# Kernel optimization log

Measured on AMD Instinct MI355X. Metric: run time of the kernel, lower is better.

## Reference

```python
import jax, jax.numpy as jnp
import numpy as np

N = 50000      # n_nodes
E = 800000     # n_edges (avg degree 16)
D_IN, D_HID, D_OUT = 128, 128, 64


def setup_inputs() -> dict:
    key = jax.random.key(0)
    ks = jax.random.split(key, 6)
    x = jax.random.normal(ks[0], (N, D_IN), dtype=jnp.float32)
    edge_index = jax.random.randint(ks[1], (2, E), 0, N, dtype=jnp.int32)
    # GCNConv params (glorot-ish scale), bias enabled by default in PyG
    W1 = jax.random.normal(ks[2], (D_IN, D_HID), dtype=jnp.float32) * (1.0 / np.sqrt(D_IN))
    b1 = jnp.zeros((D_HID,), dtype=jnp.float32)
    W2 = jax.random.normal(ks[3], (D_HID, D_OUT), dtype=jnp.float32) * (1.0 / np.sqrt(D_HID))
    b2 = jnp.zeros((D_OUT,), dtype=jnp.float32)
    return {"x": x, "edge_index": edge_index, "W1": W1, "b1": b1, "W2": W2, "b2": b2}


def _gcn_conv(x, src, dst, W, b):
    """PyG GCNConv: linear transform, add self-loops (weight 1),
    symmetric D^-1/2 A D^-1/2 aggregation (source->target), add bias."""
    xw = x @ W                                                # [N, Dout]
    ones = jnp.ones(dst.shape[0], dtype=xw.dtype)
    deg = jax.ops.segment_sum(ones, dst, num_segments=N) + 1.0  # +1 self-loop
    dis = jax.lax.rsqrt(deg)                                  # deg >= 1
    norm = dis[src] * dis[dst]                                # [E]
    msg = xw[src] * norm[:, None]                             # gather + scale
    agg = jax.ops.segment_sum(msg, dst, num_segments=N)       # scatter-add
    agg = agg + xw * (dis * dis)[:, None]                     # self-loop term
    return agg + b


def reference(x, edge_index, W1, b1, W2, b2):
    src, dst = edge_index[0], edge_index[1]
    z = jax.nn.relu(_gcn_conv(x, src, dst, W1, b1))
    z = _gcn_conv(z, src, dst, W2, b2)
    return z
```

## Files before the change

### kernel.cpp

```cpp
#include <hip/hip_runtime.h>

#define NN 50000
#define NE 800000
#define NB 196
#define BCAP 4608
#define KPAD 136
#define WSLAB (2 * 64 * KPAD)
#define CHUNKS 782
#define G1A 391
#define NBF 256

typedef __bf16 bf16x8 __attribute__((ext_vector_type(8)));
typedef float  f32x4  __attribute__((ext_vector_type(4)));

static __device__ __forceinline__ float bf2f(unsigned short h){
  union { unsigned u; float f; } c; c.u = ((unsigned)h) << 16; return c.f;
}
static __device__ __forceinline__ unsigned short f2bf(float f){
  union { float f; unsigned u; } c; c.f = f;
  unsigned u = c.u;
  return (unsigned short)((u + 0x7fffu + ((u >> 16) & 1u)) >> 16);
}
static __device__ __forceinline__ void split8(const float* f, bf16x8& hi, bf16x8& lo){
  #pragma unroll
  for (int j = 0; j < 8; j++){
    __bf16 h = (__bf16)f[j];
    hi[j] = h;
    lo[j] = (__bf16)(f[j] - (float)h);
  }
}
static __device__ __forceinline__ void addu4s(float* a, uint4 w, float s){
  a[0] = fmaf(s, bf2f((unsigned short)(w.x & 0xffffu)), a[0]);
  a[1] = fmaf(s, bf2f((unsigned short)(w.x >> 16)),     a[1]);
  a[2] = fmaf(s, bf2f((unsigned short)(w.y & 0xffffu)), a[2]);
  a[3] = fmaf(s, bf2f((unsigned short)(w.y >> 16)),     a[3]);
  a[4] = fmaf(s, bf2f((unsigned short)(w.z & 0xffffu)), a[4]);
  a[5] = fmaf(s, bf2f((unsigned short)(w.z >> 16)),     a[5]);
  a[6] = fmaf(s, bf2f((unsigned short)(w.w & 0xffffu)), a[6]);
  a[7] = fmaf(s, bf2f((unsigned short)(w.w >> 16)),     a[7]);
}
static __device__ __forceinline__ void addu4(float* a, uint4 w){
  a[0] += bf2f((unsigned short)(w.x & 0xffffu)); a[1] += bf2f((unsigned short)(w.x >> 16));
  a[2] += bf2f((unsigned short)(w.y & 0xffffu)); a[3] += bf2f((unsigned short)(w.y >> 16));
  a[4] += bf2f((unsigned short)(w.z & 0xffffu)); a[5] += bf2f((unsigned short)(w.z >> 16));
  a[6] += bf2f((unsigned short)(w.w & 0xffffu)); a[7] += bf2f((unsigned short)(w.w >> 16));
}

static __device__ __forceinline__ void gemm1_body(int chunk, int t,
    const float* __restrict__ X, const unsigned short* __restrict__ wbuf,
    unsigned short* __restrict__ Y){
  const int wv = t >> 6;
  const int lane = t & 63;
  const int m = lane & 15;
  const int quad = lane >> 4;
  const int R0 = chunk * 64;
  const int row = R0 + wv * 16 + m;
  const int rowc = min(row, NN - 1);
  const float* pX = X + (size_t)rowc * 128 + quad * 8;

  f32x4 acc[8];
  #pragma unroll
  for (int tt = 0; tt < 8; tt++) acc[tt] = (f32x4){0.f, 0.f, 0.f, 0.f};

  #pragma unroll
  for (int ki = 0; ki < 4; ki++){
    float a[8];
    *(float4*)(a)     = *(const float4*)(pX + ki * 32);
    *(float4*)(a + 4) = *(const float4*)(pX + ki * 32 + 4);
    bf16x8 ah, al;
    split8(a, ah, al);
    #pragma unroll
    for (int tt = 0; tt < 8; tt++){
      const unsigned short* bp = wbuf + (tt >> 2) * WSLAB
                               + ((tt & 3) * 16 + m) * KPAD + ki * 32 + quad * 8;
      bf16x8 bh = *(const bf16x8*)bp;
      bf16x8 bl = *(const bf16x8*)(bp + 64 * KPAD);
      acc[tt] = __builtin_amdgcn_mfma_f32_16x16x32_bf16(ah, bh, acc[tt], 0, 0, 0);
      acc[tt] = __builtin_amdgcn_mfma_f32_16x16x32_bf16(ah, bl, acc[tt], 0, 0, 0);
      acc[tt] = __builtin_amdgcn_mfma_f32_16x16x32_bf16(al, bh, acc[tt], 0, 0, 0);
    }
  }

  const int orow = R0 + wv * 16 + quad * 4;
  #pragma unroll
  for (int r = 0; r < 4; r++){
    int gr = orow + r;
    if (gr < NN){
      #pragma unroll
      for (int tt = 0; tt < 8; tt++)
        Y[(size_t)gr * 128 + (tt >> 2) * 64 + (tt & 3) * 16 + m] = f2bf(acc[tt][r]);
    }
  }
}

__global__ __launch_bounds__(256) void k_prep(const float* __restrict__ W1,
    const float* __restrict__ W2, unsigned short* __restrict__ wbuf,
    int* __restrict__ gcur){
  int s = blockIdx.x;
  if (s == 3){
    if (threadIdx.x < NB) gcur[threadIdx.x] = 0;
    return;
  }
  const float* W = (s < 2) ? W1 : W2;
  int ldw = (s < 2) ? 128 : 64;
  int coff = (s == 1) ? 64 : 0;
  unsigned short* wh = wbuf + (size_t)s * WSLAB;
  unsigned short* wl = wh + 64 * KPAD;
  for (int i = threadIdx.x; i < 128 * 64; i += 256){
    int k = i >> 6, n = i & 63;
    float v = W[(size_t)k * ldw + coff + n];
    unsigned short h = f2bf(v);
    unsigned short l = f2bf(v - bf2f(h));
    wh[n * KPAD + k] = h;
    wl[n * KPAD + k] = l;
  }
}

__global__ __launch_bounds__(256) void k_fg1(const int* __restrict__ src,
    const int* __restrict__ dst, int* __restrict__ gcur, unsigned* __restrict__ stg,
    const float* __restrict__ X, const unsigned short* __restrict__ wbuf,
    unsigned short* __restrict__ Y){
  const int bid = blockIdx.x;
  const int t = threadIdx.x;
  if (bid >= NBF){
    gemm1_body(bid - NBF, t, X, wbuf, Y);
    return;
  }
  __shared__ int lcnt[NB];
  __shared__ int gbase[NB];
  for (int i = t; i < NB; i += 256) lcnt[i] = 0;
  __syncthreads();
  const int per = (NE + NBF - 1) / NBF;
  const int e0 = bid * per, e1 = min(e0 + per, NE);
  for (int e = e0 + t; e < e1; e += 256)
    atomicAdd(&lcnt[dst[e] >> 8], 1);
  __syncthreads();
  for (int b = t; b < NB; b += 256){
    gbase[b] = atomicAdd(&gcur[b], lcnt[b]);
    lcnt[b] = 0;
  }
  __syncthreads();
  for (int e = e0 + t; e < e1; e += 256){
    int d = dst[e];
    int b = d >> 8;
    unsigned entry = (unsigned)src[e] | (((unsigned)d & 255u) << 16);
    int pos = gbase[b] + atomicAdd(&lcnt[b], 1);
    if (pos < BCAP) stg[(size_t)b * BCAP + pos] = entry;
  }
}

__global__ __launch_bounds__(256) void k_bg1(const unsigned* __restrict__ stg,
    const int* __restrict__ gcur, int* __restrict__ rowstart, int* __restrict__ cnt,
    float* __restrict__ dis, int* __restrict__ csr,
    const float* __restrict__ X, const unsigned short* __restrict__ wbuf,
    unsigned short* __restrict__ Y){
  const int bid = blockIdx.x;
  const int t = threadIdx.x;
  if (bid >= NB){
    gemm1_body(G1A + (bid - NB), t, X, wbuf, Y);
    return;
  }
  __shared__ int lcnt[256];
  __shared__ int sm[256];
  const int b = bid;
  const int ecnt = min(gcur[b], BCAP);
  const int ebase = b * BCAP;
  lcnt[t] = 0;
  __syncthreads();
  for (int i = t; i < ecnt; i += 256){
    unsigned en = stg[ebase + i];
    atomicAdd(&lcnt[(en >> 16) & 255u], 1);
  }
  __syncthreads();
  int v = lcnt[t];
  sm[t] = v;
  __syncthreads();
  #pragma unroll
  for (int off = 1; off < 256; off <<= 1){
    int x = (t >= off) ? sm[t - off] : 0;
    __syncthreads();
    sm[t] += x;
    __syncthreads();
  }
  const int loff = sm[t] - v;
  const int node = (b << 8) + t;
  if (node < NN){
    rowstart[node] = ebase + loff;
    cnt[node] = v;
    dis[node] = rsqrtf((float)v + 1.0f);
  }
  __syncthreads();
  lcnt[t] = loff;
  __syncthreads();
  for (int i = t; i < ecnt; i += 256){
    unsigned en = stg[ebase + i];
    int pos = atomicAdd(&lcnt[(en >> 16) & 255u], 1);
    csr[ebase + pos] = (int)(en & 0xffffu);
  }
}

__global__ __launch_bounds__(256) void k_agg1(const unsigned short* __restrict__ Y,
    const int* __restrict__ rowstart, const int* __restrict__ cnt,
    const int* __restrict__ csr, const float* __restrict__ dis,
    const float* __restrict__ bias, unsigned short* __restrict__ OH){
  const int n = (blockIdx.x * 256 + threadIdx.x) >> 6;
  const int lane = threadIdx.x & 63;
  const int q = lane >> 4;
  const int l = lane & 15;
  if (n >= NN) return;
  const float dn = dis[n];
  float a[8] = {0.f, 0.f, 0.f, 0.f, 0.f, 0.f, 0.f, 0.f};
  if (q == 0)
    addu4s(a, *(const uint4*)(Y + (size_t)n * 128 + (l << 3)), dn);
  const int start = rowstart[n];
  const int end = start + cnt[n];
  int i = start;
  for (; i + 16 <= end; i += 16){
    int s0 = csr[i + q],     s1 = csr[i + 4 + q];
    int s2 = csr[i + 8 + q], s3 = csr[i + 12 + q];
    float d0 = dis[s0], d1 = dis[s1], d2 = dis[s2], d3 = dis[s3];
    uint4 w0 = *(const uint4*)(Y + (size_t)s0 * 128 + (l << 3));
    uint4 w1 = *(const uint4*)(Y + (size_t)s1 * 128 + (l << 3));
    uint4 w2 = *(const uint4*)(Y + (size_t)s2 * 128 + (l << 3));
    uint4 w3 = *(const uint4*)(Y + (size_t)s3 * 128 + (l << 3));
    addu4s(a, w0, d0); addu4s(a, w1, d1); addu4s(a, w2, d2); addu4s(a, w3, d3);
  }
  for (; i + 8 <= end; i += 8){
    int s0 = csr[i + q], s1 = csr[i + 4 + q];
    float d0 = dis[s0], d1 = dis[s1];
    uint4 w0 = *(const uint4*)(Y + (size_t)s0 * 128 + (l << 3));
    uint4 w1 = *(const uint4*)(Y + (size_t)s1 * 128 + (l << 3));
    addu4s(a, w0, d0); addu4s(a, w1, d1);
  }
  for (; i < end; i += 4){
    int idx = i + q;
    if (idx < end){
      int s = csr[idx];
      addu4s(a, *(const uint4*)(Y + (size_t)s * 128 + (l << 3)), dis[s]);
    }
  }
  #pragma unroll
  for (int j = 0; j < 8; j++){
    a[j] += __shfl_xor(a[j], 16);
    a[j] += __shfl_xor(a[j], 32);
  }
  if (q == 0){
    float bi[8];
    *(float4*)(bi)     = *(const float4*)(bias + (l << 3));
    *(float4*)(bi + 4) = *(const float4*)(bias + (l << 3) + 4);
    unsigned hv[4];
    #pragma unroll
    for (int j = 0; j < 4; j++){
      float o0 = fmaxf(dn * a[2 * j]     + bi[2 * j],     0.f);
      float o1 = fmaxf(dn * a[2 * j + 1] + bi[2 * j + 1], 0.f);
      hv[j] = (unsigned)f2bf(o0) | ((unsigned)f2bf(o1) << 16);
    }
    *(uint4*)(OH + (size_t)n * 128 + (l << 3)) = make_uint4(hv[0], hv[1], hv[2], hv[3]);
  }
}

__global__ __launch_bounds__(256) void k_gemm2(const unsigned short* __restrict__ Ah,
    const unsigned short* __restrict__ Wsl, const float* __restrict__ dis,
    unsigned short* __restrict__ Y){
  const int t = threadIdx.x;
  const int wv = t >> 6;
  const int lane = t & 63;
  const int m = lane & 15;
  const int quad = lane >> 4;
  const int R0 = blockIdx.x * 64;
  const int row = R0 + wv * 16 + m;
  const int rowc = min(row, NN - 1);
  const unsigned short* pAh = Ah + (size_t)rowc * 128 + quad * 8;

  f32x4 acc[4];
  #pragma unroll
  for (int tt = 0; tt < 4; tt++) acc[tt] = (f32x4){0.f, 0.f, 0.f, 0.f};

  #pragma unroll
  for (int ki = 0; ki < 4; ki++){
    bf16x8 ah = *(const bf16x8*)(pAh + ki * 32);
    #pragma unroll
    for (int tt = 0; tt < 4; tt++){
      const unsigned short* bp = Wsl + (tt * 16 + m) * KPAD + ki * 32 + quad * 8;
      bf16x8 bh = *(const bf16x8*)bp;
      bf16x8 bl = *(const bf16x8*)(bp + 64 * KPAD);
      acc[tt] = __builtin_amdgcn_mfma_f32_16x16x32_bf16(ah, bh, acc[tt], 0, 0, 0);
      acc[tt] = __builtin_amdgcn_mfma_f32_16x16x32_bf16(ah, bl, acc[tt], 0, 0, 0);
    }
  }

  const int orow = R0 + wv * 16 + quad * 4;
  #pragma unroll
  for (int r = 0; r < 4; r++){
    int gr = orow + r;
    if (gr < NN){
      float dsc = dis[gr];
      #pragma unroll
      for (int tt = 0; tt < 4; tt++)
        Y[(size_t)gr * 64 + tt * 16 + m] = f2bf(acc[tt][r] * dsc);
    }
  }
}

__global__ __launch_bounds__(256) void k_agg64(const unsigned short* __restrict__ Y,
    const int* __restrict__ rowstart, const int* __restrict__ cnt,
    const int* __restrict__ csr, const float* __restrict__ dis,
    const float* __restrict__ bias, float* __restrict__ OUT){
  const int n = (blockIdx.x * 256 + threadIdx.x) >> 6;
  const int lane = threadIdx.x & 63;
  const int g = lane >> 3;
  const int l = lane & 7;
  if (n >= NN) return;
  float a[8] = {0.f, 0.f, 0.f, 0.f, 0.f, 0.f, 0.f, 0.f};
  if (g == 0)
    addu4(a, *(const uint4*)(Y + (size_t)n * 64 + (l << 3)));
  const int start = rowstart[n];
  const int end = start + cnt[n];
  int i = start;
  for (; i + 16 <= end; i += 16){
    int s0 = csr[i + g], s1 = csr[i + 8 + g];
    uint4 w0 = *(const uint4*)(Y + (size_t)s0 * 64 + (l << 3));
    uint4 w1 = *(const uint4*)(Y + (size_t)s1 * 64 + (l << 3));
    addu4(a, w0); addu4(a, w1);
  }
  for (; i < end; i += 8){
    int idx = i + g;
    if (idx < end){
      int s = csr[idx];
      addu4(a, *(const uint4*)(Y + (size_t)s * 64 + (l << 3)));
    }
  }
  #pragma unroll
  for (int j = 0; j < 8; j++){
    a[j] += __shfl_xor(a[j], 8);
    a[j] += __shfl_xor(a[j], 16);
    a[j] += __shfl_xor(a[j], 32);
  }
  if (g == 0){
    const float dn = dis[n];
    float bi[8];
    *(float4*)(bi)     = *(const float4*)(bias + (l << 3));
    *(float4*)(bi + 4) = *(const float4*)(bias + (l << 3) + 4);
    float4 o0, o1;
    o0.x = dn * a[0] + bi[0]; o0.y = dn * a[1] + bi[1];
    o0.z = dn * a[2] + bi[2]; o0.w = dn * a[3] + bi[3];
    o1.x = dn * a[4] + bi[4]; o1.y = dn * a[5] + bi[5];
    o1.z = dn * a[6] + bi[6]; o1.w = dn * a[7] + bi[7];
    *(float4*)(OUT + (size_t)n * 64 + (l << 3))     = o0;
    *(float4*)(OUT + (size_t)n * 64 + (l << 3) + 4) = o1;
  }
}

extern "C" void kernel_launch(void* const* d_in, const int* in_sizes, int n_in,
                              void* d_out, int out_size, void* d_ws, size_t ws_size,
                              hipStream_t stream) {
  const float* x  = (const float*)d_in[0];
  const int*   ei = (const int*)d_in[1];
  const int*   src = ei;
  const int*   dst = ei + NE;
  const float* W1 = (const float*)d_in[2];
  const float* b1 = (const float*)d_in[3];
  const float* W2 = (const float*)d_in[4];
  const float* b2 = (const float*)d_in[5];
  float* out = (float*)d_out;

  char* w = (char*)d_ws;
  auto alloc = [&](size_t bytes){ void* p = (void*)w; w += (bytes + 255) & ~(size_t)255; return p; };
  int*   gcur     = (int*)alloc(NB * 4);
  int*   rowstart = (int*)alloc((size_t)NN * 4);
  int*   cnt      = (int*)alloc((size_t)NN * 4);
  float* dis      = (float*)alloc((size_t)NN * 4);
  unsigned* stg   = (unsigned*)alloc((size_t)NB * BCAP * 4);
  int*   csr      = (int*)alloc((size_t)NB * BCAP * 4);
  unsigned short* y1 = (unsigned short*)alloc((size_t)NN * 128 * 2);
  unsigned short* hh = (unsigned short*)alloc((size_t)NN * 128 * 2);
  unsigned short* y2 = (unsigned short*)alloc((size_t)NN * 64 * 2);
  unsigned short* wbuf = (unsigned short*)alloc((size_t)3 * WSLAB * 2);

  const int AGG_BLOCKS = (NN * 64 + 255) / 256;
  unsigned short* wsl2 = wbuf + (size_t)2 * WSLAB;

  k_prep<<<4, 256, 0, stream>>>(W1, W2, wbuf, gcur);
  k_fg1 <<<NBF + G1A, 256, 0, stream>>>(src, dst, gcur, stg, x, wbuf, y1);
  k_bg1 <<<NB + (CHUNKS - G1A), 256, 0, stream>>>(stg, gcur, rowstart, cnt, dis, csr,
                                                  x, wbuf, y1);
  k_agg1 <<<AGG_BLOCKS, 256, 0, stream>>>(y1, rowstart, cnt, csr, dis, b1, hh);
  k_gemm2<<<CHUNKS, 256, 0, stream>>>(hh, wsl2, dis, y2);
  k_agg64<<<AGG_BLOCKS, 256, 0, stream>>>(y2, rowstart, cnt, csr, dis, b2, out);
}
```

Baseline: 196.2 us.

## Fuse layer-1 aggregation into layer-2 GEMM via shared-memory tile

Merges the first-layer neighbor aggregation (with bias and ReLU) and the second-layer MFMA GEMM into one kernel. Each block aggregates 64 nodes into a bf16 tile in LDS, then runs the GEMM straight from LDS. This removes one launch and the global write and read of the 50000x128 hidden buffer. In exchange the grid drops to 782 blocks, each doing 16 serial aggregation iterations per wave, which reduces parallelism and latency hiding for the gather-heavy aggregation.

```diff
diff --git a/kernel.cpp b/kernel.cpp
--- a/kernel.cpp
+++ b/kernel.cpp
@@ -199,86 +199,92 @@
   }
 }
 
-__global__ __launch_bounds__(256) void k_agg1(const unsigned short* __restrict__ Y,
+__global__ __launch_bounds__(256) void k_aggemm2(const unsigned short* __restrict__ Y,
     const int* __restrict__ rowstart, const int* __restrict__ cnt,
     const int* __restrict__ csr, const float* __restrict__ dis,
-    const float* __restrict__ bias, unsigned short* __restrict__ OH){
-  const int n = (blockIdx.x * 256 + threadIdx.x) >> 6;
-  const int lane = threadIdx.x & 63;
-  const int q = lane >> 4;
-  const int l = lane & 15;
-  if (n >= NN) return;
-  const float dn = dis[n];
-  float a[8] = {0.f, 0.f, 0.f, 0.f, 0.f, 0.f, 0.f, 0.f};
-  if (q == 0)
-    addu4s(a, *(const uint4*)(Y + (size_t)n * 128 + (l << 3)), dn);
-  const int start = rowstart[n];
-  const int end = start + cnt[n];
-  int i = start;
-  for (; i + 16 <= end; i += 16){
-    int s0 = csr[i + q],     s1 = csr[i + 4 + q];
-    int s2 = csr[i + 8 + q], s3 = csr[i + 12 + q];
-    float d0 = dis[s0], d1 = dis[s1], d2 = dis[s2], d3 = dis[s3];
-    uint4 w0 = *(const uint4*)(Y + (size_t)s0 * 128 + (l << 3));
-    uint4 w1 = *(const uint4*)(Y + (size_t)s1 * 128 + (l << 3));
-    uint4 w2 = *(const uint4*)(Y + (size_t)s2 * 128 + (l << 3));
-    uint4 w3 = *(const uint4*)(Y + (size_t)s3 * 128 + (l << 3));
-    addu4s(a, w0, d0); addu4s(a, w1, d1); addu4s(a, w2, d2); addu4s(a, w3, d3);
-  }
-  for (; i + 8 <= end; i += 8){
-    int s0 = csr[i + q], s1 = csr[i + 4 + q];
-    float d0 = dis[s0], d1 = dis[s1];
-    uint4 w0 = *(const uint4*)(Y + (size_t)s0 * 128 + (l << 3));
-    uint4 w1 = *(const uint4*)(Y + (size_t)s1 * 128 + (l << 3));
-    addu4s(a, w0, d0); addu4s(a, w1, d1);
-  }
-  for (; i < end; i += 4){
-    int idx = i + q;
-    if (idx < end){
-      int s = csr[idx];
-      addu4s(a, *(const uint4*)(Y + (size_t)s * 128 + (l << 3)), dis[s]);
-    }
-  }
-  #pragma unroll
-  for (int j = 0; j < 8; j++){
-    a[j] += __shfl_xor(a[j], 16);
-    a[j] += __shfl_xor(a[j], 32);
-  }
-  if (q == 0){
-    float bi[8];
-    *(float4*)(bi)     = *(const float4*)(bias + (l << 3));
-    *(float4*)(bi + 4) = *(const float4*)(bias + (l << 3) + 4);
-    unsigned hv[4];
-    #pragma unroll
-    for (int j = 0; j < 4; j++){
-      float o0 = fmaxf(dn * a[2 * j]     + bi[2 * j],     0.f);
-      float o1 = fmaxf(dn * a[2 * j + 1] + bi[2 * j + 1], 0.f);
-      hv[j] = (unsigned)f2bf(o0) | ((unsigned)f2bf(o1) << 16);
-    }
-    *(uint4*)(OH + (size_t)n * 128 + (l << 3)) = make_uint4(hv[0], hv[1], hv[2], hv[3]);
-  }
-}
-
-__global__ __launch_bounds__(256) void k_gemm2(const unsigned short* __restrict__ Ah,
-    const unsigned short* __restrict__ Wsl, const float* __restrict__ dis,
-    unsigned short* __restrict__ Y){
+    const float* __restrict__ bias, const unsigned short* __restrict__ Wsl,
+    unsigned short* __restrict__ Y2){
+  __shared__ unsigned short hbuf[64 * KPAD];
   const int t = threadIdx.x;
   const int wv = t >> 6;
   const int lane = t & 63;
-  const int m = lane & 15;
-  const int quad = lane >> 4;
+  const int q = lane >> 4;
+  const int l = lane & 15;
   const int R0 = blockIdx.x * 64;
-  const int row = R0 + wv * 16 + m;
-  const int rowc = min(row, NN - 1);
-  const unsigned short* pAh = Ah + (size_t)rowc * 128 + quad * 8;
-
+
+  float bi[8];
+  if (q == 0){
+    *(float4*)(bi)     = *(const float4*)(bias + (l << 3));
+    *(float4*)(bi + 4) = *(const float4*)(bias + (l << 3) + 4);
+  }
+
+  #pragma unroll 1
+  for (int it = 0; it < 16; it++){
+    const int nl = it * 4 + wv;
+    const int n = R0 + nl;
+    if (n < NN){
+      const float dn = dis[n];
+      float a[8] = {0.f, 0.f, 0.f, 0.f, 0.f, 0.f, 0.f, 0.f};
+      if (q == 0)
+        addu4s(a, *(const uint4*)(Y + (size_t)n * 128 + (l << 3)), dn);
+      const int start = rowstart[n];
+      const int end = start + cnt[n];
+      int i = start;
+      for (; i + 16 <= end; i += 16){
+        int s0 = csr[i + q],     s1 = csr[i + 4 + q];
+        int s2 = csr[i + 8 + q], s3 = csr[i + 12 + q];
+        float d0 = dis[s0], d1 = dis[s1], d2 = dis[s2], d3 = dis[s3];
+        uint4 w0 = *(const uint4*)(Y + (size_t)s0 * 128 + (l << 3));
+        uint4 w1 = *(const uint4*)(Y + (size_t)s1 * 128 + (l << 3));
+        uint4 w2 = *(const uint4*)(Y + (size_t)s2 * 128 + (l << 3));
+        uint4 w3 = *(const uint4*)(Y + (size_t)s3 * 128 + (l << 3));
+        addu4s(a, w0, d0); addu4s(a, w1, d1); addu4s(a, w2, d2); addu4s(a, w3, d3);
+      }
+      for (; i + 8 <= end; i += 8){
+        int s0 = csr[i + q], s1 = csr[i + 4 + q];
+        float d0 = dis[s0], d1 = dis[s1];
+        uint4 w0 = *(const uint4*)(Y + (size_t)s0 * 128 + (l << 3));
+        uint4 w1 = *(const uint4*)(Y + (size_t)s1 * 128 + (l << 3));
+        addu4s(a, w0, d0); addu4s(a, w1, d1);
+      }
+      for (; i < end; i += 4){
+        int idx = i + q;
+        if (idx < end){
+          int s = csr[idx];
+          addu4s(a, *(const uint4*)(Y + (size_t)s * 128 + (l << 3)), dis[s]);
+        }
+      }
+      #pragma unroll
+      for (int j = 0; j < 8; j++){
+        a[j] += __shfl_xor(a[j], 16);
+        a[j] += __shfl_xor(a[j], 32);
+      }
+      if (q == 0){
+        unsigned hv[4];
+        #pragma unroll
+        for (int j = 0; j < 4; j++){
+          float o0 = fmaxf(dn * a[2 * j]     + bi[2 * j],     0.f);
+          float o1 = fmaxf(dn * a[2 * j + 1] + bi[2 * j + 1], 0.f);
+          hv[j] = (unsigned)f2bf(o0) | ((unsigned)f2bf(o1) << 16);
+        }
+        *(uint4*)(hbuf + nl * KPAD + (l << 3)) = make_uint4(hv[0], hv[1], hv[2], hv[3]);
+      }
+    } else {
+      if (q == 0)
+        *(uint4*)(hbuf + nl * KPAD + (l << 3)) = make_uint4(0u, 0u, 0u, 0u);
+    }
+  }
+  __syncthreads();
+
+  const int m = l;
+  const int quad = q;
   f32x4 acc[4];
   #pragma unroll
   for (int tt = 0; tt < 4; tt++) acc[tt] = (f32x4){0.f, 0.f, 0.f, 0.f};
 
   #pragma unroll
   for (int ki = 0; ki < 4; ki++){
-    bf16x8 ah = *(const bf16x8*)(pAh + ki * 32);
+    bf16x8 ah = *(const bf16x8*)(hbuf + (wv * 16 + m) * KPAD + ki * 32 + quad * 8);
     #pragma unroll
     for (int tt = 0; tt < 4; tt++){
       const unsigned short* bp = Wsl + (tt * 16 + m) * KPAD + ki * 32 + quad * 8;
@@ -297,7 +303,7 @@
       float dsc = dis[gr];
       #pragma unroll
       for (int tt = 0; tt < 4; tt++)
-        Y[(size_t)gr * 64 + tt * 16 + m] = f2bf(acc[tt][r] * dsc);
+        Y2[(size_t)gr * 64 + tt * 16 + m] = f2bf(acc[tt][r] * dsc);
     }
   }
 }
@@ -373,7 +379,6 @@
   unsigned* stg   = (unsigned*)alloc((size_t)NB * BCAP * 4);
   int*   csr      = (int*)alloc((size_t)NB * BCAP * 4);
   unsigned short* y1 = (unsigned short*)alloc((size_t)NN * 128 * 2);
-  unsigned short* hh = (unsigned short*)alloc((size_t)NN * 128 * 2);
   unsigned short* y2 = (unsigned short*)alloc((size_t)NN * 64 * 2);
   unsigned short* wbuf = (unsigned short*)alloc((size_t)3 * WSLAB * 2);
 
@@ -384,7 +389,6 @@
   k_fg1 <<<NBF + G1A, 256, 0, stream>>>(src, dst, gcur, stg, x, wbuf, y1);
   k_bg1 <<<NB + (CHUNKS - G1A), 256, 0, stream>>>(stg, gcur, rowstart, cnt, dis, csr,
                                                   x, wbuf, y1);
-  k_agg1 <<<AGG_BLOCKS, 256, 0, stream>>>(y1, rowstart, cnt, csr, dis, b1, hh);
-  k_gemm2<<<CHUNKS, 256, 0, stream>>>(hh, wsl2, dis, y2);
+  k_aggemm2<<<CHUNKS, 256, 0, stream>>>(y1, rowstart, cnt, csr, dis, b1, wsl2, y2);
   k_agg64<<<AGG_BLOCKS, 256, 0, stream>>>(y2, rowstart, cnt, csr, dis, b2, out);
 }
```

Measured after the change: 210.2 us. 1.07x slower.
